# Kernel optimization log

Measured on AMD Instinct MI355X. Metric: run time of the kernel, lower is better.

## Reference

```python
import jax, jax.numpy as jnp
import numpy as np

L = 2048
E = 1024
H = 16
D = E // H


def setup_inputs() -> dict:
    key = jax.random.key(0)
    ks = jax.random.split(key, 9)
    inp = {
        "values": jax.random.normal(ks[0], (L, E), dtype=jnp.float32),
        "keys": jax.random.normal(ks[1], (L, E), dtype=jnp.float32),
        "query": jax.random.normal(ks[2], (L, E), dtype=jnp.float32),
        "dist_matrix": jax.random.uniform(ks[3], (L, L), dtype=jnp.float32),
        "Wv": jax.random.normal(ks[4], (E, E), dtype=jnp.float32) * 0.02,
        "Wk": jax.random.normal(ks[5], (E, E), dtype=jnp.float32) * 0.02,
        "Wq": jax.random.normal(ks[6], (E, E), dtype=jnp.float32) * 0.02,
        "Wo": jax.random.normal(ks[7], (E, E), dtype=jnp.float32) * 0.02,
        "bo": jax.random.normal(ks[8], (E,), dtype=jnp.float32) * 0.02,
    }
    return inp


def reference(values, keys, query, dist_matrix, Wv, Wk, Wq, Wo, bo):
    # Linear projections (torch Linear: x @ W.T), then split heads: [L, H, D]
    v = (values @ Wv.T).reshape(L, H, D)
    k = (keys @ Wk.T).reshape(L, H, D)
    q = (query @ Wq.T).reshape(L, H, D)

    # energy: [H, Lq, Lk]
    energy = jnp.einsum("qhd,khd->hqk", q, k)

    # distance bias: zeros -> inf, then 1/(d+1); broadcast over heads
    dm = jnp.where(dist_matrix == 0, jnp.inf, dist_matrix)
    bias = 1.0 / (dm + 1.0)
    energy = energy + bias[None, :, :]

    attn = jax.nn.softmax(energy / jnp.sqrt(jnp.float32(E)), axis=2)

    out = jnp.einsum("hql,lhd->qhd", attn, v).reshape(L, H * D)
    return out @ Wo.T + bo
```

## Files before the change

### kernel.cpp

```cpp
#include <hip/hip_runtime.h>


#define L_SEQ 2048
#define E_DIM 1024
#define H_HEADS 16
#define D_HEAD 64
#define KSPLIT 4

typedef unsigned short u16;
typedef unsigned int u32;
typedef __attribute__((ext_vector_type(8))) short bf16x8;
typedef __attribute__((ext_vector_type(8))) unsigned short u16x8;
typedef __attribute__((ext_vector_type(4))) unsigned short u16x4;
typedef __attribute__((ext_vector_type(4))) float f32x4;

#define C_LOG2E_32 0.045084220027780106f

__device__ __forceinline__ float bf2f(u16 u) {
  union { u32 i; float f; } v; v.i = ((u32)u) << 16; return v.f;
}
__device__ __forceinline__ u16 f2bf(float f) {
  union { float f; u32 i; } v; v.f = f;
  u32 u = v.i;
  u += 0x7FFFu + ((u >> 16) & 1u);
  return (u16)(u >> 16);
}
__device__ __forceinline__ u32 pack_bf16_pair(float lo, float hi) {
  union { float f; u32 u; } a, b;
  a.f = lo; b.f = hi;
  return __builtin_amdgcn_perm(b.u + 0x8000u, a.u + 0x8000u, 0x07060302u);
}
__device__ __forceinline__ void gload16(const u16* g, u16* l) {
  __builtin_amdgcn_global_load_lds(
      (const __attribute__((address_space(1))) u32*)g,
      (__attribute__((address_space(3))) u32*)l, 16, 0, 0);
}

__global__ void cvt_all(const float* __restrict__ xq, const float* __restrict__ xk,
                        const float* __restrict__ xv,
                        const float* __restrict__ wq, const float* __restrict__ wk,
                        const float* __restrict__ wv, const float* __restrict__ wo,
                        const float* __restrict__ dist,
                        u16* oq, u16* ok, u16* ov,
                        u16* owq, u16* owk, u16* owv, u16* owo, u16* obias)
{
  size_t gid = (size_t)blockIdx.x * 256 + threadIdx.x;
  const size_t NQ = 524288;
  const size_t NW = 262144;
  const float* src; u16* dst; size_t off; bool isb = false;
  if      (gid <     NQ)           { src = xq;   dst = oq;    off = gid; }
  else if (gid < 2 * NQ)           { src = xk;   dst = ok;    off = gid - NQ; }
  else if (gid < 3 * NQ)           { src = xv;   dst = ov;    off = gid - 2 * NQ; }
  else if (gid < 3 * NQ + NW)      { src = wq;   dst = owq;   off = gid - 3 * NQ; }
  else if (gid < 3 * NQ + 2 * NW)  { src = wk;   dst = owk;   off = gid - 3 * NQ - NW; }
  else if (gid < 3 * NQ + 3 * NW)  { src = wv;   dst = owv;   off = gid - 3 * NQ - 2 * NW; }
  else if (gid < 3 * NQ + 4 * NW)  { src = wo;   dst = owo;   off = gid - 3 * NQ - 3 * NW; }
  else { src = dist; dst = obias; off = gid - 3 * NQ - 4 * NW; isb = true; }

  f32x4 v = *(const f32x4*)&src[off * 4];
  u16x4 o;
#pragma unroll
  for (int j = 0; j < 4; ++j) {
    float f = v[j];
    if (isb) f = (f == 0.f) ? 0.f : C_LOG2E_32 / (f + 1.f);
    o[j] = f2bf(f);
  }
  *(u16x4*)&dst[off * 4] = o;
}

__global__ void bias_fill(const float* __restrict__ bo, float* __restrict__ out)
{
  size_t gid = (size_t)blockIdx.x * 256 + threadIdx.x;
  int n = (int)((gid * 4) & (E_DIM - 1));
  *(f32x4*)&out[gid * 4] = *(const f32x4*)&bo[n];
}

#define TM 128
#define TN 128
#define BK 64

template<int OUTMODE>
__global__ __launch_bounds__(256, 2) void gemm_bt3c(
    const u16* __restrict__ A0, const u16* __restrict__ B0, void* __restrict__ C0,
    const u16* __restrict__ A1, const u16* __restrict__ B1, void* __restrict__ C1,
    const u16* __restrict__ A2, const u16* __restrict__ B2, void* __restrict__ C2,
    int M, int N, int K)
{
  const u16* A; const u16* B; void* C;
  if (OUTMODE == 2)         { A = A0; B = B0; C = C0; }
  else if (blockIdx.z == 0) { A = A0; B = B0; C = C0; }
  else if (blockIdx.z == 1) { A = A1; B = B1; C = C1; }
  else                      { A = A2; B = B2; C = C2; }

  __shared__ __align__(16) u16 As[TM * BK];
  __shared__ __align__(16) u16 Bs[TN * BK];

  const int m0 = blockIdx.y * TM;
  const int n0 = blockIdx.x * TN;
  const int t = threadIdx.x;
  const int wave = t >> 6;
  const int lane = t & 63;
  const int quad = lane >> 4;
  const int col  = lane & 15;
  const int wm = (wave >> 1) * 64;
  const int wn = (wave & 1) * 64;

  const int roff = lane >> 3;
  const int gcol = ((lane & 7) ^ roff) * 8;
  const u16* gA = A + (size_t)(m0 + wave * 32 + roff) * K + gcol;
  const u16* gB = B + (size_t)(n0 + wave * 32 + roff) * K + gcol;

  const int kbeg = (OUTMODE == 2) ? blockIdx.z * (K / KSPLIT) : 0;
  const int kend = (OUTMODE == 2) ? kbeg + K / KSPLIT : K;

  f32x4 acc[4][4];
#pragma unroll
  for (int i = 0; i < 4; ++i)
#pragma unroll
    for (int j = 0; j < 4; ++j) acc[i][j] = (f32x4){0.f, 0.f, 0.f, 0.f};

  const int c7 = col & 7;

  for (int k0 = kbeg; k0 < kend; k0 += BK) {
    __syncthreads();
#pragma unroll
    for (int s = 0; s < 4; ++s) {
      gload16(gA + (size_t)(s * 8) * K + k0, &As[(wave * 32 + s * 8) * BK]);
      gload16(gB + (size_t)(s * 8) * K + k0, &Bs[(wave * 32 + s * 8) * BK]);
    }
    __syncthreads();

    bf16x8 af[4][2], bfr[4][2];
#pragma unroll
    for (int ks = 0; ks < 2; ++ks) {
      const int slot = ((ks * 4 + quad) ^ c7) * 8;
#pragma unroll
      for (int i = 0; i < 4; ++i)
        af[i][ks] = *(const bf16x8*)&As[(wm + i * 16 + col) * BK + slot];
#pragma unroll
      for (int j = 0; j < 4; ++j)
        bfr[j][ks] = *(const bf16x8*)&Bs[(wn + j * 16 + col) * BK + slot];
    }

#pragma unroll
    for (int ks = 0; ks < 2; ++ks)
#pragma unroll
      for (int i = 0; i < 4; ++i)
#pragma unroll
        for (int j = 0; j < 4; ++j)
          acc[i][j] = __builtin_amdgcn_mfma_f32_16x16x32_bf16(af[i][ks], bfr[j][ks], acc[i][j], 0, 0, 0);
  }

  const bool transC = (OUTMODE == 0) && (blockIdx.z == 2);
#pragma unroll
  for (int i = 0; i < 4; ++i) {
    int rowb = m0 + wm + i * 16 + quad * 4;
#pragma unroll
    for (int j = 0; j < 4; ++j) {
      int cn = n0 + wn + j * 16 + col;
      if (OUTMODE == 2) {
#pragma unroll
        for (int r = 0; r < 4; ++r)
          unsafeAtomicAdd(&((float*)C)[(size_t)(rowb + r) * N + cn], acc[i][j][r]);
      } else if (transC) {
        u16x4 pk;
#pragma unroll
        for (int r = 0; r < 4; ++r) pk[r] = f2bf(acc[i][j][r]);
        *(u16x4*)&((u16*)C)[(size_t)cn * M + rowb] = pk;
      } else {
#pragma unroll
        for (int r = 0; r < 4; ++r)
          ((u16*)C)[(size_t)(rowb + r) * N + cn] = f2bf(acc[i][j][r]);
      }
    }
  }
}

#define FK 64
#define LDV 72

__global__ __launch_bounds__(256, 5) void flash3(
    const u16* __restrict__ Q, const u16* __restrict__ Kp,
    const u16* __restrict__ Vt, const u16* __restrict__ Bb,
    u16* __restrict__ Op, float* __restrict__ lp)
{
  __shared__ __align__(16) u16 Ks[FK][LDV];
  __shared__ __align__(16) u16 Vs[D_HEAD][LDV];
  __shared__ __align__(16) u16 Ps[4][16][LDV];

  const int h  = blockIdx.y;
  const int q0 = blockIdx.x * 64;
  const int z  = blockIdx.z;
  const int hoff = h * D_HEAD;
  const int kbase = z * (L_SEQ / KSPLIT);
  const int t = threadIdx.x;
  const int wave = t >> 6;
  const int lane = t & 63;
  const int quad = lane >> 4;
  const int col  = lane & 15;

  bf16x8 qf[2];
  {
    const u16* qrow = Q + (size_t)(q0 + wave * 16 + col) * E_DIM + hoff;
    qf[0] = *(const bf16x8*)(qrow + quad * 8);
    qf[1] = *(const bf16x8*)(qrow + 32 + quad * 8);
  }

  float l_lane = 0.f;
  f32x4 oacc[4];
#pragma unroll
  for (int td = 0; td < 4; ++td) oacc[td] = (f32x4){0.f, 0.f, 0.f, 0.f};

  const u16* brow = Bb + (size_t)(q0 + wave * 16 + col) * L_SEQ;
  const int cst = t & 7, rst = t >> 3;

  for (int kt = 0; kt < L_SEQ / KSPLIT / FK; ++kt) {
    const int k0 = kbase + kt * FK;
    __syncthreads();
#pragma unroll
    for (int s = 0; s < 2; ++s) {
      int rr = rst + s * 32;
      *(u16x8*)&Ks[rr][cst * 8] = *(const u16x8*)&Kp[(size_t)(k0 + rr) * E_DIM + hoff + cst * 8];
      *(u16x8*)&Vs[rr][cst * 8] = *(const u16x8*)&Vt[(size_t)(hoff + rr) * L_SEQ + k0 + cst * 8];
    }
    float pb[4][4];
#pragma unroll
    for (int tt = 0; tt < 4; ++tt) {
      u16x4 bv = *(const u16x4*)&brow[k0 + tt * 16 + quad * 4];
#pragma unroll
      for (int r = 0; r < 4; ++r) pb[tt][r] = bf2f(bv[r]);
    }
    __syncthreads();

#pragma unroll
    for (int tt = 0; tt < 4; ++tt) {
      f32x4 a = (f32x4){0.f, 0.f, 0.f, 0.f};
      a = __builtin_amdgcn_mfma_f32_16x16x32_bf16(*(const bf16x8*)&Ks[tt * 16 + col][quad * 8], qf[0], a, 0, 0, 0);
      a = __builtin_amdgcn_mfma_f32_16x16x32_bf16(*(const bf16x8*)&Ks[tt * 16 + col][32 + quad * 8], qf[1], a, 0, 0, 0);
      float p[4];
#pragma unroll
      for (int r = 0; r < 4; ++r) {
        p[r] = __builtin_amdgcn_exp2f(fmaf(a[r], C_LOG2E_32, pb[tt][r]));
        l_lane += p[r];
      }
      uint2 w;
      w.x = pack_bf16_pair(p[0], p[1]);
      w.y = pack_bf16_pair(p[2], p[3]);
      *(uint2*)&Ps[wave][col][tt * 16 + quad * 4] = w;
    }

#pragma unroll
    for (int kk = 0; kk < 2; ++kk) {
      bf16x8 pf = *(const bf16x8*)&Ps[wave][col][kk * 32 + quad * 8];
#pragma unroll
      for (int td = 0; td < 4; ++td) {
        bf16x8 vf = *(const bf16x8*)&Vs[td * 16 + col][kk * 32 + quad * 8];
        oacc[td] = __builtin_amdgcn_mfma_f32_16x16x32_bf16(pf, vf, oacc[td], 0, 0, 0);
      }
    }
  }

  l_lane += __shfl_xor(l_lane, 16);
  l_lane += __shfl_xor(l_lane, 32);
  if (lane < 16)
    lp[((size_t)z * L_SEQ + q0 + wave * 16 + lane) * H_HEADS + h] = l_lane;

  const int qrow_mine = q0 + wave * 16 + quad * 4;
#pragma unroll
  for (int td = 0; td < 4; ++td)
#pragma unroll
    for (int r = 0; r < 4; ++r)
      Op[((size_t)z * L_SEQ + qrow_mine + r) * E_DIM + hoff + td * 16 + col] = f2bf(oacc[td][r]);
}

__global__ void merge_attn(const u16* __restrict__ Op, const float* __restrict__ lp,
                           u16* __restrict__ AOb)
{
  size_t gid = (size_t)blockIdx.x * 256 + threadIdx.x;
  size_t idx = gid * 4;
  int q = (int)(idx >> 10);
  int e = (int)(idx & 1023);
  int h = e >> 6;
  float o[4] = {0.f, 0.f, 0.f, 0.f};
  float lsum = 0.f;
#pragma unroll
  for (int s = 0; s < KSPLIT; ++s) {
    u16x4 pv = *(const u16x4*)&Op[((size_t)s * L_SEQ + q) * E_DIM + e];
#pragma unroll
    for (int j = 0; j < 4; ++j) o[j] += bf2f(pv[j]);
    lsum += lp[((size_t)s * L_SEQ + q) * H_HEADS + h];
  }
  float inv = 1.f / lsum;
  u16x4 pk;
#pragma unroll
  for (int j = 0; j < 4; ++j) pk[j] = f2bf(o[j] * inv);
  *(u16x4*)&AOb[idx] = pk;
}

extern "C" void kernel_launch(void* const* d_in, const int* in_sizes, int n_in,
                              void* d_out, int out_size, void* d_ws, size_t ws_size,
                              hipStream_t stream)
{
  const float* values = (const float*)d_in[0];
  const float* keys   = (const float*)d_in[1];
  const float* query  = (const float*)d_in[2];
  const float* dist   = (const float*)d_in[3];
  const float* Wv     = (const float*)d_in[4];
  const float* Wk     = (const float*)d_in[5];
  const float* Wq     = (const float*)d_in[6];
  const float* Wo     = (const float*)d_in[7];
  const float* bo     = (const float*)d_in[8];
  float* out = (float*)d_out;

  const size_t MB = (size_t)1 << 20;
  char* w = (char*)d_ws;
  u16* xq  = (u16*)(w + 0 * MB);
  u16* xk  = (u16*)(w + 4 * MB);
  u16* xv  = (u16*)(w + 8 * MB);
  u16* wqb = (u16*)(w + 12 * MB);
  u16* wkb = (u16*)(w + 14 * MB);
  u16* wvb = (u16*)(w + 16 * MB);
  u16* wob = (u16*)(w + 18 * MB);
  u16* Bb  = (u16*)(w + 20 * MB);
  u16* Qh  = (u16*)(w + 28 * MB);
  u16* Kh  = (u16*)(w + 32 * MB);
  u16* Vth = (u16*)(w + 36 * MB);
  u16* AOb = (u16*)(w + 40 * MB);
  float* lp = (float*)(w + 44 * MB);
  u16* Op  = (u16*)(w + 0 * MB);

  cvt_all<<<14336, 256, 0, stream>>>(query, keys, values, Wq, Wk, Wv, Wo, dist,
                                     xq, xk, xv, wqb, wkb, wvb, wob, Bb);

  bias_fill<<<(L_SEQ * E_DIM / 4) / 256, 256, 0, stream>>>(bo, out);

  dim3 gProj(E_DIM / TN, L_SEQ / TM, 3);
  gemm_bt3c<0><<<gProj, 256, 0, stream>>>(xq, wqb, Qh,
                                          xk, wkb, Kh,
                                          xv, wvb, Vth,
                                          L_SEQ, E_DIM, E_DIM);

  dim3 gAttn(L_SEQ / 64, H_HEADS, KSPLIT);
  flash3<<<gAttn, 256, 0, stream>>>(Qh, Kh, Vth, Bb, Op, lp);

  merge_attn<<<(L_SEQ * E_DIM / 4) / 256, 256, 0, stream>>>(Op, lp, AOb);

  dim3 gOut(E_DIM / TN, L_SEQ / TM, KSPLIT);
  gemm_bt3c<2><<<gOut, 256, 0, stream>>>(AOb, wob, out,
                                         AOb, wob, out,
                                         AOb, wob, out,
                                         L_SEQ, E_DIM, E_DIM);
}
```

Baseline: 223.0 us.

## Double-buffer GEMM loads, keep P in registers for PV MFMA, fuse bias fill

The projection/output GEMM now uses BK=32 with two LDS buffers, prefetching the next K tile while computing the current one. This removes one barrier per iteration and raises occupancy hints. Flash attention feeds the exp'd probabilities straight into 16x16x16 bf16 MFMAs (P as B operand) instead of round-tripping through LDS, and the output layout is transposed accordingly. The bias_fill launch is merged into the conversion kernel, and the output GEMM split-K drops from 4 to 2, trading atomic traffic for fewer blocks.

New measurement: 221.8 us. Within noise of the previous version (-0.5%).

```diff
diff --git a/kernel.cpp b/kernel.cpp
--- a/kernel.cpp
+++ b/kernel.cpp
@@ -6,15 +6,23 @@
 #define H_HEADS 16
 #define D_HEAD 64
 #define KSPLIT 4
+#define OSPLIT 2
 
 typedef unsigned short u16;
 typedef unsigned int u32;
 typedef __attribute__((ext_vector_type(8))) short bf16x8;
+typedef __attribute__((ext_vector_type(4))) short bf16x4;
 typedef __attribute__((ext_vector_type(8))) unsigned short u16x8;
 typedef __attribute__((ext_vector_type(4))) unsigned short u16x4;
 typedef __attribute__((ext_vector_type(4))) float f32x4;
 
 #define C_LOG2E_32 0.045084220027780106f
+
+#if __has_builtin(__builtin_amdgcn_mfma_f32_16x16x16bf16_1k)
+#define HAVE_MFMA16 1
+#else
+#define HAVE_MFMA16 0
+#endif
 
 __device__ __forceinline__ float bf2f(u16 u) {
   union { u32 i; float f; } v; v.i = ((u32)u) << 16; return v.f;
@@ -40,13 +48,24 @@
                         const float* __restrict__ xv,
                         const float* __restrict__ wq, const float* __restrict__ wk,
                         const float* __restrict__ wv, const float* __restrict__ wo,
-                        const float* __restrict__ dist,
+                        const float* __restrict__ dist, const float* __restrict__ bo,
                         u16* oq, u16* ok, u16* ov,
-                        u16* owq, u16* owk, u16* owv, u16* owo, u16* obias)
+                        u16* owq, u16* owk, u16* owv, u16* owo, u16* obias,
+                        float* __restrict__ outp)
 {
   size_t gid = (size_t)blockIdx.x * 256 + threadIdx.x;
   const size_t NQ = 524288;
   const size_t NW = 262144;
+  const size_t DL = 1048576;
+  const size_t FILL = 3 * NQ + 4 * NW + DL;
+
+  if (gid >= FILL) {
+    size_t off = (gid - FILL) * 4;
+    int n = (int)(off & (E_DIM - 1));
+    *(f32x4*)&outp[off] = *(const f32x4*)&bo[n];
+    return;
+  }
+
   const float* src; u16* dst; size_t off; bool isb = false;
   if      (gid <     NQ)           { src = xq;   dst = oq;    off = gid; }
   else if (gid < 2 * NQ)           { src = xk;   dst = ok;    off = gid - NQ; }
@@ -68,19 +87,12 @@
   *(u16x4*)&dst[off * 4] = o;
 }
 
-__global__ void bias_fill(const float* __restrict__ bo, float* __restrict__ out)
-{
-  size_t gid = (size_t)blockIdx.x * 256 + threadIdx.x;
-  int n = (int)((gid * 4) & (E_DIM - 1));
-  *(f32x4*)&out[gid * 4] = *(const f32x4*)&bo[n];
-}
-
 #define TM 128
 #define TN 128
-#define BK 64
+#define BK 32
 
 template<int OUTMODE>
-__global__ __launch_bounds__(256, 2) void gemm_bt3c(
+__global__ __launch_bounds__(256, 3) void gemm_pd(
     const u16* __restrict__ A0, const u16* __restrict__ B0, void* __restrict__ C0,
     const u16* __restrict__ A1, const u16* __restrict__ B1, void* __restrict__ C1,
     const u16* __restrict__ A2, const u16* __restrict__ B2, void* __restrict__ C2,
@@ -92,8 +104,8 @@
   else if (blockIdx.z == 1) { A = A1; B = B1; C = C1; }
   else                      { A = A2; B = B2; C = C2; }
 
-  __shared__ __align__(16) u16 As[TM * BK];
-  __shared__ __align__(16) u16 Bs[TN * BK];
+  __shared__ __align__(16) u16 As[2][TM * BK];
+  __shared__ __align__(16) u16 Bs[2][TN * BK];
 
   const int m0 = blockIdx.y * TM;
   const int n0 = blockIdx.x * TN;
@@ -105,13 +117,15 @@
   const int wm = (wave >> 1) * 64;
   const int wn = (wave & 1) * 64;
 
-  const int roff = lane >> 3;
-  const int gcol = ((lane & 7) ^ roff) * 8;
+  const int roff = lane >> 2;
+  const int gcol = ((lane & 3) ^ ((lane >> 3) & 3)) * 8;
   const u16* gA = A + (size_t)(m0 + wave * 32 + roff) * K + gcol;
   const u16* gB = B + (size_t)(n0 + wave * 32 + roff) * K + gcol;
-
-  const int kbeg = (OUTMODE == 2) ? blockIdx.z * (K / KSPLIT) : 0;
-  const int kend = (OUTMODE == 2) ? kbeg + K / KSPLIT : K;
+  const int lo0 = (wave * 32) * BK;
+  const int lo1 = (wave * 32 + 16) * BK;
+
+  const int kbeg = (OUTMODE == 2) ? blockIdx.z * (K / OSPLIT) : 0;
+  const int kend = (OUTMODE == 2) ? kbeg + K / OSPLIT : K;
 
   f32x4 acc[4][4];
 #pragma unroll
@@ -119,36 +133,39 @@
 #pragma unroll
     for (int j = 0; j < 4; ++j) acc[i][j] = (f32x4){0.f, 0.f, 0.f, 0.f};
 
-  const int c7 = col & 7;
-
+  gload16(gA + kbeg, &As[0][lo0]);
+  gload16(gA + (size_t)16 * K + kbeg, &As[0][lo1]);
+  gload16(gB + kbeg, &Bs[0][lo0]);
+  gload16(gB + (size_t)16 * K + kbeg, &Bs[0][lo1]);
+
+  const int slot8 = (quad ^ ((col >> 1) & 3)) * 8;
+
+  int buf = 0;
   for (int k0 = kbeg; k0 < kend; k0 += BK) {
     __syncthreads();
-#pragma unroll
-    for (int s = 0; s < 4; ++s) {
-      gload16(gA + (size_t)(s * 8) * K + k0, &As[(wave * 32 + s * 8) * BK]);
-      gload16(gB + (size_t)(s * 8) * K + k0, &Bs[(wave * 32 + s * 8) * BK]);
-    }
-    __syncthreads();
-
-    bf16x8 af[4][2], bfr[4][2];
-#pragma unroll
-    for (int ks = 0; ks < 2; ++ks) {
-      const int slot = ((ks * 4 + quad) ^ c7) * 8;
-#pragma unroll
-      for (int i = 0; i < 4; ++i)
-        af[i][ks] = *(const bf16x8*)&As[(wm + i * 16 + col) * BK + slot];
+    int nk = k0 + BK;
+    if (nk < kend) {
+      gload16(gA + nk, &As[buf ^ 1][lo0]);
+      gload16(gA + (size_t)16 * K + nk, &As[buf ^ 1][lo1]);
+      gload16(gB + nk, &Bs[buf ^ 1][lo0]);
+      gload16(gB + (size_t)16 * K + nk, &Bs[buf ^ 1][lo1]);
+    }
+
+    bf16x8 af[4], bfr[4];
+#pragma unroll
+    for (int i = 0; i < 4; ++i)
+      af[i] = *(const bf16x8*)&As[buf][(wm + i * 16 + col) * BK + slot8];
+#pragma unroll
+    for (int j = 0; j < 4; ++j)
+      bfr[j] = *(const bf16x8*)&Bs[buf][(wn + j * 16 + col) * BK + slot8];
+
+#pragma unroll
+    for (int i = 0; i < 4; ++i)
 #pragma unroll
       for (int j = 0; j < 4; ++j)
-        bfr[j][ks] = *(const bf16x8*)&Bs[(wn + j * 16 + col) * BK + slot];
-    }
-
-#pragma unroll
-    for (int ks = 0; ks < 2; ++ks)
-#pragma unroll
-      for (int i = 0; i < 4; ++i)
-#pragma unroll
-        for (int j = 0; j < 4; ++j)
-          acc[i][j] = __builtin_amdgcn_mfma_f32_16x16x32_bf16(af[i][ks], bfr[j][ks], acc[i][j], 0, 0, 0);
+        acc[i][j] = __builtin_amdgcn_mfma_f32_16x16x32_bf16(af[i], bfr[j], acc[i][j], 0, 0, 0);
+
+    buf ^= 1;
   }
 
   const bool transC = (OUTMODE == 0) && (blockIdx.z == 2);
@@ -179,14 +196,16 @@
 #define FK 64
 #define LDV 72
 
-__global__ __launch_bounds__(256, 5) void flash3(
+__global__ __launch_bounds__(256, 6) void flash4(
     const u16* __restrict__ Q, const u16* __restrict__ Kp,
     const u16* __restrict__ Vt, const u16* __restrict__ Bb,
     u16* __restrict__ Op, float* __restrict__ lp)
 {
   __shared__ __align__(16) u16 Ks[FK][LDV];
   __shared__ __align__(16) u16 Vs[D_HEAD][LDV];
+#if !HAVE_MFMA16
   __shared__ __align__(16) u16 Ps[4][16][LDV];
+#endif
 
   const int h  = blockIdx.y;
   const int q0 = blockIdx.x * 64;
@@ -243,12 +262,24 @@
         p[r] = __builtin_amdgcn_exp2f(fmaf(a[r], C_LOG2E_32, pb[tt][r]));
         l_lane += p[r];
       }
+#if HAVE_MFMA16
+      union { u32 u[2]; bf16x4 v; } pk;
+      pk.u[0] = pack_bf16_pair(p[0], p[1]);
+      pk.u[1] = pack_bf16_pair(p[2], p[3]);
+#pragma unroll
+      for (int td = 0; td < 4; ++td) {
+        bf16x4 vf = *(const bf16x4*)&Vs[td * 16 + col][tt * 16 + quad * 4];
+        oacc[td] = __builtin_amdgcn_mfma_f32_16x16x16bf16_1k(vf, pk.v, oacc[td], 0, 0, 0);
+      }
+#else
       uint2 w;
       w.x = pack_bf16_pair(p[0], p[1]);
       w.y = pack_bf16_pair(p[2], p[3]);
       *(uint2*)&Ps[wave][col][tt * 16 + quad * 4] = w;
-    }
-
+#endif
+    }
+
+#if !HAVE_MFMA16
 #pragma unroll
     for (int kk = 0; kk < 2; ++kk) {
       bf16x8 pf = *(const bf16x8*)&Ps[wave][col][kk * 32 + quad * 8];
@@ -258,6 +289,7 @@
         oacc[td] = __builtin_amdgcn_mfma_f32_16x16x32_bf16(pf, vf, oacc[td], 0, 0, 0);
       }
     }
+#endif
   }
 
   l_lane += __shfl_xor(l_lane, 16);
@@ -265,12 +297,23 @@
   if (lane < 16)
     lp[((size_t)z * L_SEQ + q0 + wave * 16 + lane) * H_HEADS + h] = l_lane;
 
+#if HAVE_MFMA16
+  const int qmine = q0 + wave * 16 + col;
+#pragma unroll
+  for (int td = 0; td < 4; ++td) {
+    u16x4 pk;
+#pragma unroll
+    for (int r = 0; r < 4; ++r) pk[r] = f2bf(oacc[td][r]);
+    *(u16x4*)&Op[((size_t)z * L_SEQ + qmine) * E_DIM + hoff + td * 16 + quad * 4] = pk;
+  }
+#else
   const int qrow_mine = q0 + wave * 16 + quad * 4;
 #pragma unroll
   for (int td = 0; td < 4; ++td)
 #pragma unroll
     for (int r = 0; r < 4; ++r)
       Op[((size_t)z * L_SEQ + qrow_mine + r) * E_DIM + hoff + td * 16 + col] = f2bf(oacc[td][r]);
+#endif
 }
 
 __global__ void merge_attn(const u16* __restrict__ Op, const float* __restrict__ lp,
@@ -329,25 +372,23 @@
   float* lp = (float*)(w + 44 * MB);
   u16* Op  = (u16*)(w + 0 * MB);
 
-  cvt_all<<<14336, 256, 0, stream>>>(query, keys, values, Wq, Wk, Wv, Wo, dist,
-                                     xq, xk, xv, wqb, wkb, wvb, wob, Bb);
-
-  bias_fill<<<(L_SEQ * E_DIM / 4) / 256, 256, 0, stream>>>(bo, out);
+  cvt_all<<<16384, 256, 0, stream>>>(query, keys, values, Wq, Wk, Wv, Wo, dist, bo,
+                                     xq, xk, xv, wqb, wkb, wvb, wob, Bb, out);
 
   dim3 gProj(E_DIM / TN, L_SEQ / TM, 3);
-  gemm_bt3c<0><<<gProj, 256, 0, stream>>>(xq, wqb, Qh,
-                                          xk, wkb, Kh,
-                                          xv, wvb, Vth,
-                                          L_SEQ, E_DIM, E_DIM);
+  gemm_pd<0><<<gProj, 256, 0, stream>>>(xq, wqb, Qh,
+                                        xk, wkb, Kh,
+                                        xv, wvb, Vth,
+                                        L_SEQ, E_DIM, E_DIM);
 
   dim3 gAttn(L_SEQ / 64, H_HEADS, KSPLIT);
-  flash3<<<gAttn, 256, 0, stream>>>(Qh, Kh, Vth, Bb, Op, lp);
+  flash4<<<gAttn, 256, 0, stream>>>(Qh, Kh, Vth, Bb, Op, lp);
 
   merge_attn<<<(L_SEQ * E_DIM / 4) / 256, 256, 0, stream>>>(Op, lp, AOb);
 
-  dim3 gOut(E_DIM / TN, L_SEQ / TM, KSPLIT);
-  gemm_bt3c<2><<<gOut, 256, 0, stream>>>(AOb, wob, out,
-                                         AOb, wob, out,
-                                         AOb, wob, out,
-                                         L_SEQ, E_DIM, E_DIM);
-}
+  dim3 gOut(E_DIM / TN, L_SEQ / TM, OSPLIT);
+  gemm_pd<2><<<gOut, 256, 0, stream>>>(AOb, wob, out,
+                                       AOb, wob, out,
+                                       AOb, wob, out,
+                                       L_SEQ, E_DIM, E_DIM);
+}
```
